# Optimization experiments

Hardware: AMD Instinct MI355X
Metric: run time of the kernel (lower is better)

## Reference

```python
import jax, jax.numpy as jnp
import numpy as np


def setup_inputs() -> dict:
    key = jax.random.key(0)
    ks = jax.random.split(key, 9)
    B, C, H, W = 8, 512, 56, 56
    E = 256  # embed_dim = in_channels / r
    s = 0.02
    return {
        "x": jax.random.normal(ks[0], (B, C, H, W), dtype=jnp.float32),
        "wq": jax.random.normal(ks[1], (E, C), dtype=jnp.float32) * s,
        "bq": jax.random.normal(ks[2], (E,), dtype=jnp.float32) * s,
        "wk": jax.random.normal(ks[3], (E, C), dtype=jnp.float32) * s,
        "bk": jax.random.normal(ks[4], (E,), dtype=jnp.float32) * s,
        "wv": jax.random.normal(ks[5], (E, C), dtype=jnp.float32) * s,
        "bv": jax.random.normal(ks[6], (E,), dtype=jnp.float32) * s,
        "wo": jax.random.normal(ks[7], (C, E), dtype=jnp.float32) * s,
        "bo": jax.random.normal(ks[8], (C,), dtype=jnp.float32) * s,
    }


def reference(x, wq, bq, wk, bk, wv, bv, wo, bo):
    B, C, H, W = x.shape
    N = H * W
    # 1x1 convs == per-pixel linear projections; flatten spatial dims
    xf = x.reshape(B, C, N)                                   # b c n
    q = jnp.einsum("ec,bcn->bne", wq, xf) + bq                # b n e
    k = jnp.einsum("ec,bcn->ben", wk, xf) + bk[None, :, None] # b e n
    v = jnp.einsum("ec,bcn->bne", wv, xf) + bv                # b n e
    attn = jnp.einsum("bne,bem->bnm", q, k) / N               # b n n (unnormalized, /N scale)
    embed = jnp.einsum("bnm,bme->bne", attn, v)               # b n e
    out = jnp.einsum("ce,bne->bcn", wo, embed) + bo[None, :, None]
    return out.reshape(B, C, H, W) + x
```

## Files before the change

kernel.cpp:

```cpp
#include <hip/hip_runtime.h>
#include <hip/hip_bf16.h>


typedef __attribute__((ext_vector_type(8))) __bf16 bf16x8;
typedef __attribute__((ext_vector_type(8))) short s16x8;
typedef __attribute__((ext_vector_type(4))) float floatx4;

struct __align__(8) bh4 { __hip_bfloat16 x, y, z, w; };
struct __align__(16) bh8 { __hip_bfloat16 h[8]; };

__device__ __forceinline__ void load_lds16(const void* g, void* l) {
    __builtin_amdgcn_global_load_lds((const __attribute__((address_space(1))) void*)g,
                                     (__attribute__((address_space(3))) void*)l, 16, 0, 0);
}

__global__ __launch_bounds__(256)
void prep_trans(const float* __restrict__ x, __hip_bfloat16* __restrict__ xnp,
                float* __restrict__ s,
                const float* __restrict__ wo, const float* __restrict__ wv,
                const float* __restrict__ wq, const float* __restrict__ wk,
                const float* __restrict__ bq, const float* __restrict__ bk,
                const float* __restrict__ bv,
                __hip_bfloat16* __restrict__ Pdb, __hip_bfloat16* __restrict__ Qtb,
                float* __restrict__ u, float* __restrict__ r, float* __restrict__ w,
                float* __restrict__ kap)
{
    __shared__ __align__(16) float smem[2 * 16 * 68];
    const int tid = threadIdx.x;

    if (blockIdx.z == 8) {
        const int blk = blockIdx.y * 50 + blockIdx.x;
        if (blk >= 130) return;
        if (blk >= 128) {
            int c = (blk - 128) * 256 + tid;
            float su = 0.f, sr = 0.f, sw = 0.f;
            for (int e = 0; e < 256; ++e) {
                su = fmaf(wo[(long long)c * 256 + e], bv[e], su);
                sr = fmaf(bk[e], wq[(long long)e * 512 + c], sr);
                sw = fmaf(wk[(long long)e * 512 + c], bq[e], sw);
            }
            u[c] = su; r[c] = sr; w[c] = sw;
            if (c == 0) {
                float k2 = 0.f;
                for (int e = 0; e < 256; ++e) k2 = fmaf(bk[e], bq[e], k2);
                *kap = k2;
            }
            return;
        }
        const bool doQ = (blk >= 64);
        const int tt = blk & 63;
        const int m0 = (tt >> 3) * 64, n0 = (tt & 7) * 64;
        float (*As)[68] = (float(*)[68])smem;
        float (*Bs)[68] = (float(*)[68])(smem + 16 * 68);
        const int tx = tid & 15, ty = tid >> 4;
        const int lk = tid >> 4, lc = (tid & 15) * 4;
        const int lr = tid >> 2, lk4 = (tid & 3) * 4;
        float acc[4][4] = {};
        for (int k0 = 0; k0 < 256; k0 += 16) {
            float4 av, bv4;
            if (doQ) {
                av = *(const float4*)&wq[(long long)(k0 + lk) * 512 + m0 + lc];
                bv4 = *(const float4*)&wk[(long long)(k0 + lk) * 512 + n0 + lc];
            } else {
                av = *(const float4*)&wo[(long long)(m0 + lr) * 256 + k0 + lk4];
                bv4 = *(const float4*)&wv[(long long)(k0 + lk) * 512 + n0 + lc];
            }
            __syncthreads();
            if (doQ) {
                *(float4*)&As[lk][lc] = av;
            } else {
                As[lk4 + 0][lr] = av.x; As[lk4 + 1][lr] = av.y;
                As[lk4 + 2][lr] = av.z; As[lk4 + 3][lr] = av.w;
            }
            *(float4*)&Bs[lk][lc] = bv4;
            __syncthreads();
#pragma unroll
            for (int kk = 0; kk < 16; ++kk) {
                float a[4], b[4];
#pragma unroll
                for (int i = 0; i < 4; ++i) { a[i] = As[kk][ty * 4 + i]; b[i] = Bs[kk][tx * 4 + i]; }
#pragma unroll
                for (int i = 0; i < 4; ++i)
#pragma unroll
                    for (int j = 0; j < 4; ++j) acc[i][j] = fmaf(a[i], b[j], acc[i][j]);
            }
        }
        const int mo = m0 + ty * 4, no = n0 + tx * 4;
        if (doQ) {
#pragma unroll
            for (int i = 0; i < 4; ++i)
#pragma unroll
                for (int j = 0; j < 4; ++j)
                    Qtb[(long long)(mo + i) * 512 + no + j] = __float2bfloat16(acc[i][j]);
        } else {
#pragma unroll
            for (int i = 0; i < 4; ++i)
#pragma unroll
                for (int j = 0; j < 4; ++j) {
                    __hip_bfloat16 v = __float2bfloat16(acc[i][j]);
                    Pdb[(long long)(mo + i) * 1024 + no + j] = v;
                    Pdb[(long long)(mo + i) * 1024 + no + j + 512] = v;
                }
        }
        return;
    }

    const int b = blockIdx.z;
    const int n0 = blockIdx.x * 64, c0 = blockIdx.y * 64;
    const int nch = tid & 7;
    const int cr  = tid >> 3;
    __hip_bfloat16* xno = xnp + (long long)b * 512 * 3200;

    if (n0 >= 3136) {
        bh8 z8;
#pragma unroll
        for (int k = 0; k < 8; ++k) z8.h[k] = __float2bfloat16(0.f);
#pragma unroll
        for (int p = 0; p < 2; ++p)
            *(bh8*)&xno[(long long)(c0 + cr + 32 * p) * 3200 + n0 + nch * 8] = z8;
        return;
    }
    const float* xb = x + (long long)b * 512 * 3136;
    float4 v[2][2];
#pragma unroll
    for (int p = 0; p < 2; ++p) {
        const float* xr = xb + (long long)(c0 + cr + 32 * p) * 3136 + n0 + nch * 8;
        v[p][0] = *(const float4*)xr;
        v[p][1] = *(const float4*)(xr + 4);
    }
    float rsum[2];
#pragma unroll
    for (int p = 0; p < 2; ++p) {
        float4 v0 = v[p][0], v1 = v[p][1];
        bh8 o;
        o.h[0] = __float2bfloat16(v0.x); o.h[1] = __float2bfloat16(v0.y);
        o.h[2] = __float2bfloat16(v0.z); o.h[3] = __float2bfloat16(v0.w);
        o.h[4] = __float2bfloat16(v1.x); o.h[5] = __float2bfloat16(v1.y);
        o.h[6] = __float2bfloat16(v1.z); o.h[7] = __float2bfloat16(v1.w);
        *(bh8*)&xno[(long long)(c0 + cr + 32 * p) * 3200 + n0 + nch * 8] = o;
        float rs = v0.x + v0.y + v0.z + v0.w + v1.x + v1.y + v1.z + v1.w;
        rs += __shfl_xor(rs, 1, 8);
        rs += __shfl_xor(rs, 2, 8);
        rs += __shfl_xor(rs, 4, 8);
        rsum[p] = rs;
    }
    if (nch == 0) {
        atomicAdd(&s[b * 512 + c0 + cr], rsum[0]);
        atomicAdd(&s[b * 512 + c0 + cr + 32], rsum[1]);
    }
}

__global__ __launch_bounds__(256)
void vec2_kernel(const __hip_bfloat16* __restrict__ T, const __hip_bfloat16* __restrict__ Pdb,
                 const __hip_bfloat16* __restrict__ Qtb, const float* __restrict__ s,
                 const float* __restrict__ u, const float* __restrict__ w,
                 const float* __restrict__ kap, const float* __restrict__ bo,
                 float* __restrict__ ps, float* __restrict__ sq, float* __restrict__ a2)
{
    const int idx = blockIdx.x * 4 + (threadIdx.x >> 6);
    const int lane = threadIdx.x & 63;
    const int b = idx >> 9, c = idx & 511;
    const int j0 = lane * 8;
    const float* sb = s + b * 512;
    float4 s0 = *(const float4*)&sb[j0], s1 = *(const float4*)&sb[j0 + 4];
    float4 w0 = *(const float4*)&w[j0],  w1 = *(const float4*)&w[j0 + 4];
    bf16x8 pv = *(const bf16x8*)&Pdb[(long long)c * 1024 + j0];
    bf16x8 qv = *(const bf16x8*)&Qtb[(long long)c * 512 + j0];
    bf16x8 tv = *(const bf16x8*)&T[(long long)b * 262144 + (long long)c * 512 + j0];
    float sj[8] = {s0.x, s0.y, s0.z, s0.w, s1.x, s1.y, s1.z, s1.w};
    float wj[8] = {w0.x, w0.y, w0.z, w0.w, w1.x, w1.y, w1.z, w1.w};
    float aps = 0.f, asq = 0.f, atw = 0.f, asw = 0.f;
#pragma unroll
    for (int t = 0; t < 8; ++t) {
        aps = fmaf((float)pv[t], sj[t], aps);
        asq = fmaf((float)qv[t], sj[t], asq);
        atw = fmaf((float)tv[t], wj[t], atw);
        asw = fmaf(sj[t], wj[t], asw);
    }
#pragma unroll
    for (int m = 1; m < 64; m <<= 1) {
        aps += __shfl_xor(aps, m);
        asq += __shfl_xor(asq, m);
        atw += __shfl_xor(atw, m);
        asw += __shfl_xor(asw, m);
    }
    if (lane == 0) {
        ps[idx] = aps; sq[idx] = asq;
        float kp = *kap;
        a2[idx] = (atw + u[c] * asw + aps * kp) * (1.f / 3136.f) + u[c] * kp + bo[c];
    }
}

#define SWZ64(row) ((row) & 7)

__global__ __launch_bounds__(256)
void mfma_g(const __hip_bfloat16* __restrict__ A, long long sA, int lda,
            __hip_bfloat16* __restrict__ C, long long sC, int ldc,
            int kLen)
{
    constexpr int BKT = 64;
    constexpr int CPR = BKT / 8;
    constexpr int NC = 64 * CPR / 256;
    constexpr int LSZ = 64 * BKT;
    __shared__ __hip_bfloat16 As[2 * LSZ];
    __shared__ __hip_bfloat16 Bs[2 * LSZ];
    const int tid = threadIdx.x;
    const int lane = tid & 63;
    const int w = tid >> 6;
    const int wm = (w >> 1) << 5;
    const int wn = (w & 1) << 5;
    const int ln = lane & 15;
    const int hi = lane >> 4;
    const int bx = blockIdx.x;
    const int batch = bx & 7, ks = bx >> 3;
    int p = blockIdx.y, mt = 0;
    while (p >= 8 - mt) { p -= 8 - mt; ++mt; }
    const int nt = mt + p;
    const int m0 = mt << 6, n0 = nt << 6;
    const long long k0 = (long long)ks * kLen;

    const __hip_bfloat16* gA[NC];
    const __hip_bfloat16* gB[NC];
#pragma unroll
    for (int q0 = 0; q0 < NC; ++q0) {
        int q = tid + 256 * q0;
        int row = q / CPR;
        int c = (q % CPR) ^ SWZ64(row);
        gA[q0] = A + batch * sA + (long long)(m0 + row) * lda + k0 + c * 8;
        gB[q0] = A + batch * sA + (long long)(n0 + row) * lda + k0 + c * 8;
    }
    floatx4 acc[2][2] = {};
    const int nK = kLen / BKT;

#pragma unroll
    for (int q0 = 0; q0 < NC; ++q0) {
        load_lds16(gA[q0], As + (tid + 256 * q0) * 8);
        load_lds16(gB[q0], Bs + (tid + 256 * q0) * 8);
        gA[q0] += BKT; gB[q0] += BKT;
    }

    int cur = 0;
    for (int kt = 0; kt < nK; ++kt) {
        if (kt + 1 < nK) {
            const int off = (cur ^ 1) * LSZ;
#pragma unroll
            for (int q0 = 0; q0 < NC; ++q0) {
                load_lds16(gA[q0], As + off + (tid + 256 * q0) * 8);
                load_lds16(gB[q0], Bs + off + (tid + 256 * q0) * 8);
                gA[q0] += BKT; gB[q0] += BKT;
            }
            asm volatile("s_waitcnt vmcnt(4)" ::: "memory");
        } else {
            asm volatile("s_waitcnt vmcnt(0)" ::: "memory");
        }
        __builtin_amdgcn_s_barrier();
        const __hip_bfloat16* Ac = As + cur * LSZ;
        const __hip_bfloat16* Bc = Bs + cur * LSZ;
#pragma unroll
        for (int kk = 0; kk < BKT / 32; ++kk) {
            const int cidx = kk * 4 + hi;
            bf16x8 af[2], bfr[2];
#pragma unroll
            for (int i = 0; i < 2; ++i) {
                int row = wm + i * 16 + ln;
                af[i] = *(const bf16x8*)(Ac + row * BKT + ((cidx ^ SWZ64(row)) << 3));
            }
#pragma unroll
            for (int j = 0; j < 2; ++j) {
                int row = wn + j * 16 + ln;
                bfr[j] = *(const bf16x8*)(Bc + row * BKT + ((cidx ^ SWZ64(row)) << 3));
            }
#pragma unroll
            for (int i = 0; i < 2; ++i)
#pragma unroll
                for (int j = 0; j < 2; ++j)
                    acc[i][j] = __builtin_amdgcn_mfma_f32_16x16x32_bf16(af[i], bfr[j], acc[i][j], 0, 0, 0);
        }
        if (kt + 1 < nK) {
            __builtin_amdgcn_s_barrier();
            cur ^= 1;
        }
    }

    __hip_bfloat16* Cb = C + batch * sC + ks * 512;
#pragma unroll
    for (int i = 0; i < 2; ++i) {
        int mb = m0 + wm + i * 16 + hi * 4;
#pragma unroll
        for (int j = 0; j < 2; ++j) {
            int nl = n0 + wn + j * 16 + ln;
            bh4 mv;
            mv.x = __float2bfloat16(acc[i][j][0]);
            mv.y = __float2bfloat16(acc[i][j][1]);
            mv.z = __float2bfloat16(acc[i][j][2]);
            mv.w = __float2bfloat16(acc[i][j][3]);
            Cb[(long long)(mb + 0) * ldc + nl] = mv.x;
            Cb[(long long)(mb + 1) * ldc + nl] = mv.y;
            Cb[(long long)(mb + 2) * ldc + nl] = mv.z;
            Cb[(long long)(mb + 3) * ldc + nl] = mv.w;
            if (mt != nt)
                *(bh4*)&Cb[(long long)nl * ldc + mb] = mv;
        }
    }
}

template<int MODE>
__global__ __launch_bounds__(256)
void mfma_sm(const __hip_bfloat16* __restrict__ A, long long sA, int lda,
             const __hip_bfloat16* __restrict__ B, long long sB, int ldb,
             __hip_bfloat16* __restrict__ C, long long sC, int ldc,
             const float* __restrict__ pu, const float* __restrict__ pr,
             const float* __restrict__ pps, const float* __restrict__ psq,
             int kLen)
{
    constexpr int BKT = 64;
    constexpr int CPR = BKT / 8;
    constexpr int NC = 64 * CPR / 256;
    constexpr int LSZ = 64 * BKT;
    __shared__ __hip_bfloat16 As[2 * LSZ];
    __shared__ __hip_bfloat16 Bs[2 * LSZ];
    const int tid = threadIdx.x;
    const int lane = tid & 63;
    const int w = tid >> 6;
    const int wm = (w >> 1) << 5;
    const int wn = (w & 1) << 5;
    const int ln = lane & 15;
    const int hi = lane >> 4;
    const int batch = blockIdx.x;
    const int m0 = blockIdx.z << 6;
    const int n0 = blockIdx.y << 6;

    const __hip_bfloat16* gA[NC];
    const __hip_bfloat16* gB[NC];
#pragma unroll
    for (int q0 = 0; q0 < NC; ++q0) {
        int q = tid + 256 * q0;
        int row = q / CPR;
        int c = (q % CPR) ^ SWZ64(row);
        gA[q0] = A + batch * sA + (long long)(m0 + row) * lda + c * 8;
        gB[q0] = B + batch * sB + (long long)(n0 + row) * ldb + c * 8;
    }
    floatx4 acc[2][2] = {};
    const int nK = kLen / BKT;

#pragma unroll
    for (int q0 = 0; q0 < NC; ++q0) {
        load_lds16(gA[q0], As + (tid + 256 * q0) * 8);
        load_lds16(gB[q0], Bs + (tid + 256 * q0) * 8);
        gA[q0] += BKT; gB[q0] += BKT;
    }

    int cur = 0;
    for (int kt = 0; kt < nK; ++kt) {
        if (kt + 1 < nK) {
            const int off = (cur ^ 1) * LSZ;
#pragma unroll
            for (int q0 = 0; q0 < NC; ++q0) {
                load_lds16(gA[q0], As + off + (tid + 256 * q0) * 8);
                load_lds16(gB[q0], Bs + off + (tid + 256 * q0) * 8);
                gA[q0] += BKT; gB[q0] += BKT;
            }
            asm volatile("s_waitcnt vmcnt(4)" ::: "memory");
        } else {
            asm volatile("s_waitcnt vmcnt(0)" ::: "memory");
        }
        __builtin_amdgcn_s_barrier();
        const __hip_bfloat16* Ac = As + cur * LSZ;
        const __hip_bfloat16* Bc = Bs + cur * LSZ;
#pragma unroll
        for (int kk = 0; kk < BKT / 32; ++kk) {
            const int cidx = kk * 4 + hi;
            bf16x8 af[2], bfr[2];
#pragma unroll
            for (int i = 0; i < 2; ++i) {
                int row = wm + i * 16 + ln;
                af[i] = *(const bf16x8*)(Ac + row * BKT + ((cidx ^ SWZ64(row)) << 3));
            }
#pragma unroll
            for (int j = 0; j < 2; ++j) {
                int row = wn + j * 16 + ln;
                bfr[j] = *(const bf16x8*)(Bc + row * BKT + ((cidx ^ SWZ64(row)) << 3));
            }
#pragma unroll
            for (int i = 0; i < 2; ++i)
#pragma unroll
                for (int j = 0; j < 2; ++j)
                    acc[i][j] = __builtin_amdgcn_mfma_f32_16x16x32_bf16(af[i], bfr[j], acc[i][j], 0, 0, 0);
        }
        if (kt + 1 < nK) {
            __builtin_amdgcn_s_barrier();
            cur ^= 1;
        }
    }

    __hip_bfloat16* Cb = C + batch * sC;
#pragma unroll
    for (int i = 0; i < 2; ++i) {
        int mb = m0 + wm + i * 16 + hi * 4;
#pragma unroll
        for (int r = 0; r < 4; ++r) {
#pragma unroll
            for (int j = 0; j < 2; ++j) {
                int nl = n0 + wn + j * 16 + ln;
                float v = acc[i][j][r];
                if (MODE == 6) {
                    float uu = pu[mb + r], rr = pr[nl];
                    v = (v + uu * psq[batch * 512 + nl] + pps[batch * 512 + mb + r] * rr)
                        * (1.f / 3136.f) + uu * rr;
                    if (mb + r == nl) v += 1.f;
                }
                Cb[(long long)(mb + r) * ldc + nl] = __float2bfloat16(v);
            }
        }
    }
}

#define SWZB(nr) (((nr) & 7) ^ (((nr) >> 3) & 7))

__global__ __launch_bounds__(256)
void mfma64(const __hip_bfloat16* __restrict__ A, long long sA, int lda,
            const __hip_bfloat16* __restrict__ Bn, long long sB, int ldb,
            float* __restrict__ C, long long sC, int ldc,
            const float* __restrict__ bias, int sBias,
            int kLen, int Nreal)
{
    constexpr int BKT = 64;
    constexpr int CPR = BKT / 8;
    constexpr int NA = 64 * CPR / 256;
    __shared__ __hip_bfloat16 As[64 * BKT];
    __shared__ __align__(16) short Bs[128 * 64];
    const int tid = threadIdx.x;
    const int lane = tid & 63;
    const int w = tid >> 6;
    const int ln = lane & 15;
    const int hi = lane >> 4;
    const int batch = blockIdx.x;
    const int m0 = blockIdx.z << 6;
    const int n0 = blockIdx.y << 7;

    const __hip_bfloat16* gA[NA];
#pragma unroll
    for (int q0 = 0; q0 < NA; ++q0) {
        int q = tid + 256 * q0;
        int row = q / CPR;
        int c = (q % CPR) ^ SWZ64(row);
        gA[q0] = A + batch * sA + (long long)(m0 + row) * lda + c * 8;
    }
    const int bc = tid >> 2;
    const int bq = tid & 3;
    const short* bbase = (const short*)(Bn + batch * sB)
                         + (long long)bc * ldb + n0 + bq * 8;
    const int g = bc >> 3;

    floatx4 acc[4][2] = {};
    const int nK = kLen / BKT;
    for (int kt = 0; kt < nK; ++kt) {
        s16x8 vb[4];
        const short* bp = bbase + (long long)kt * 64 * ldb;
#pragma unroll
        for (int m = 0; m < 4; ++m)
            vb[m] = *(const s16x8*)(bp + m * 32);
#pragma unroll
        for (int q0 = 0; q0 < NA; ++q0) {
            load_lds16(gA[q0], As + (tid + 256 * q0) * 8);
            gA[q0] += BKT;
        }
#pragma unroll
        for (int m = 0; m < 4; ++m) {
            const int nb = (bq + 4 * m) * 8;
#pragma unroll
            for (int k = 0; k < 8; ++k) {
                const int nr = nb + k;
                Bs[nr * 64 + (((g ^ SWZB(nr)) & 7) << 3) + (bc & 7)] = vb[m][k];
            }
        }
        __syncthreads();
#pragma unroll
        for (int kk = 0; kk < BKT / 32; ++kk) {
            const int cidx = kk * 4 + hi;
            bf16x8 af[4], bfr[2];
#pragma unroll
            for (int i = 0; i < 4; ++i) {
                int row = i * 16 + ln;
                af[i] = *(const bf16x8*)(As + row * BKT + ((cidx ^ SWZ64(row)) << 3));
            }
#pragma unroll
            for (int j = 0; j < 2; ++j) {
                int row = w * 32 + j * 16 + ln;
                bfr[j] = *(const bf16x8*)((const __hip_bfloat16*)Bs
                          + row * 64 + (((cidx ^ SWZB(row)) & 7) << 3));
            }
#pragma unroll
            for (int i = 0; i < 4; ++i)
#pragma unroll
                for (int j = 0; j < 2; ++j)
                    acc[i][j] = __builtin_amdgcn_mfma_f32_16x16x32_bf16(af[i], bfr[j], acc[i][j], 0, 0, 0);
        }
        __syncthreads();
    }

    float* Cb = C + batch * sC;
#pragma unroll
    for (int i = 0; i < 4; ++i) {
        int mb = m0 + i * 16 + hi * 4;
#pragma unroll
        for (int r = 0; r < 4; ++r) {
            float bb = bias[batch * sBias + mb + r];
#pragma unroll
            for (int j = 0; j < 2; ++j) {
                int nl = n0 + w * 32 + j * 16 + ln;
                if (nl < Nreal) {
                    Cb[(long long)(mb + r) * ldc + nl] = acc[i][j][r] + bb;
                }
            }
        }
    }
}

extern "C" void kernel_launch(void* const* d_in, const int* in_sizes, int n_in,
                              void* d_out, int out_size, void* d_ws, size_t ws_size,
                              hipStream_t stream)
{
    const float* x  = (const float*)d_in[0];
    const float* wq = (const float*)d_in[1];
    const float* bq = (const float*)d_in[2];
    const float* wk = (const float*)d_in[3];
    const float* bk = (const float*)d_in[4];
    const float* wv = (const float*)d_in[5];
    const float* bv = (const float*)d_in[6];
    const float* wo = (const float*)d_in[7];
    const float* bo = (const float*)d_in[8];
    float* out = (float*)d_out;

    const int N = 3136;
    const long long xs = 512LL * N;
    const long long xs2 = 512LL * 3200;

    char* ob = (char*)d_out;
    __hip_bfloat16* Gp2 = (__hip_bfloat16*)(ob + 26214400);
    __hip_bfloat16* Tb  = (__hip_bfloat16*)(ob + 34603008);

    char* wsb = (char*)d_ws;
    __hip_bfloat16* xnp = (__hip_bfloat16*)wsb;
    __hip_bfloat16* A2b = (__hip_bfloat16*)(wsb + 26214400);
    __hip_bfloat16* Pdb = (__hip_bfloat16*)(wsb + 30408704);
    __hip_bfloat16* Qtb = (__hip_bfloat16*)(wsb + 31457280);
    float* sv  = (float*)(wsb + 31981568);
    float* u_  = (float*)(wsb + 31997952);
    float* r_  = (float*)(wsb + 32000000);
    float* w_  = (float*)(wsb + 32002048);
    float* kap = (float*)(wsb + 32004096);
    float* ps  = (float*)(wsb + 32004112);
    float* sq  = (float*)(wsb + 32020496);
    float* a2v = (float*)(wsb + 32036880);

    hipMemsetAsync(sv, 0, 512 * 8 * sizeof(float), stream);

    prep_trans<<<dim3(50, 8, 9), 256, 0, stream>>>(
        x, xnp, sv, wo, wv, wq, wk, bq, bk, bv,
        Pdb, Qtb, u_, r_, w_, kap);

    mfma_g<<<dim3(16, 36), 256, 0, stream>>>(
        xnp, xs2, 3200, Gp2, 524288, 1024, 1600);

    mfma_sm<5><<<dim3(8, 8, 8), 256, 0, stream>>>(
        Pdb, 0, 1024, Gp2, 524288, 1024, Tb, 262144, 512,
        nullptr, nullptr, nullptr, nullptr, 1024);

    vec2_kernel<<<1024, 256, 0, stream>>>(Tb, Pdb, Qtb, sv, u_, w_, kap, bo, ps, sq, a2v);

    mfma_sm<6><<<dim3(8, 8, 8), 256, 0, stream>>>(
        Tb, 262144, 512, Qtb, 0, 512, A2b, 262144, 512,
        u_, r_, ps, sq, 512);

    mfma64<<<dim3(8, 25, 8), 256, 0, stream>>>(
        A2b, 262144, 512, xnp, xs2, 3200,
        out, xs, N, a2v, 512, 512, N);
}
```

Measured before the change: 215.7 us.

## Move weight-product GEMMs from conversion kernel into Gram MFMA kernel

Drops the weight-product blocks (Wo·Wv, Wq^T·Wk and the bias vectors) from the x-conversion kernel, leaving it a pure fp32-to-bf16 transpose/convert. Those blocks now run as extra blockIdx.y rows inside the Gram MFMA kernel, sharing one LDS arena, so the weight GEMMs overlap the x-Gram compute instead of the streaming conversion. The fp32 weight GEMM also gets register prefetch of the next k-tile. The conversion kernel loses its tail imbalance, but the merged kernel gains extra blocks and may run at lower occupancy.

```diff
diff --git a/kernel.cpp b/kernel.cpp
--- a/kernel.cpp
+++ b/kernel.cpp
@@ -15,98 +15,12 @@
 }
 
 __global__ __launch_bounds__(256)
-void prep_trans(const float* __restrict__ x, __hip_bfloat16* __restrict__ xnp,
-                float* __restrict__ s,
-                const float* __restrict__ wo, const float* __restrict__ wv,
-                const float* __restrict__ wq, const float* __restrict__ wk,
-                const float* __restrict__ bq, const float* __restrict__ bk,
-                const float* __restrict__ bv,
-                __hip_bfloat16* __restrict__ Pdb, __hip_bfloat16* __restrict__ Qtb,
-                float* __restrict__ u, float* __restrict__ r, float* __restrict__ w,
-                float* __restrict__ kap)
+void conv_x(const float* __restrict__ x, __hip_bfloat16* __restrict__ xnp,
+            float* __restrict__ s)
 {
-    __shared__ __align__(16) float smem[2 * 16 * 68];
-    const int tid = threadIdx.x;
-
-    if (blockIdx.z == 8) {
-        const int blk = blockIdx.y * 50 + blockIdx.x;
-        if (blk >= 130) return;
-        if (blk >= 128) {
-            int c = (blk - 128) * 256 + tid;
-            float su = 0.f, sr = 0.f, sw = 0.f;
-            for (int e = 0; e < 256; ++e) {
-                su = fmaf(wo[(long long)c * 256 + e], bv[e], su);
-                sr = fmaf(bk[e], wq[(long long)e * 512 + c], sr);
-                sw = fmaf(wk[(long long)e * 512 + c], bq[e], sw);
-            }
-            u[c] = su; r[c] = sr; w[c] = sw;
-            if (c == 0) {
-                float k2 = 0.f;
-                for (int e = 0; e < 256; ++e) k2 = fmaf(bk[e], bq[e], k2);
-                *kap = k2;
-            }
-            return;
-        }
-        const bool doQ = (blk >= 64);
-        const int tt = blk & 63;
-        const int m0 = (tt >> 3) * 64, n0 = (tt & 7) * 64;
-        float (*As)[68] = (float(*)[68])smem;
-        float (*Bs)[68] = (float(*)[68])(smem + 16 * 68);
-        const int tx = tid & 15, ty = tid >> 4;
-        const int lk = tid >> 4, lc = (tid & 15) * 4;
-        const int lr = tid >> 2, lk4 = (tid & 3) * 4;
-        float acc[4][4] = {};
-        for (int k0 = 0; k0 < 256; k0 += 16) {
-            float4 av, bv4;
-            if (doQ) {
-                av = *(const float4*)&wq[(long long)(k0 + lk) * 512 + m0 + lc];
-                bv4 = *(const float4*)&wk[(long long)(k0 + lk) * 512 + n0 + lc];
-            } else {
-                av = *(const float4*)&wo[(long long)(m0 + lr) * 256 + k0 + lk4];
-                bv4 = *(const float4*)&wv[(long long)(k0 + lk) * 512 + n0 + lc];
-            }
-            __syncthreads();
-            if (doQ) {
-                *(float4*)&As[lk][lc] = av;
-            } else {
-                As[lk4 + 0][lr] = av.x; As[lk4 + 1][lr] = av.y;
-                As[lk4 + 2][lr] = av.z; As[lk4 + 3][lr] = av.w;
-            }
-            *(float4*)&Bs[lk][lc] = bv4;
-            __syncthreads();
-#pragma unroll
-            for (int kk = 0; kk < 16; ++kk) {
-                float a[4], b[4];
-#pragma unroll
-                for (int i = 0; i < 4; ++i) { a[i] = As[kk][ty * 4 + i]; b[i] = Bs[kk][tx * 4 + i]; }
-#pragma unroll
-                for (int i = 0; i < 4; ++i)
-#pragma unroll
-                    for (int j = 0; j < 4; ++j) acc[i][j] = fmaf(a[i], b[j], acc[i][j]);
-            }
-        }
-        const int mo = m0 + ty * 4, no = n0 + tx * 4;
-        if (doQ) {
-#pragma unroll
-            for (int i = 0; i < 4; ++i)
-#pragma unroll
-                for (int j = 0; j < 4; ++j)
-                    Qtb[(long long)(mo + i) * 512 + no + j] = __float2bfloat16(acc[i][j]);
-        } else {
-#pragma unroll
-            for (int i = 0; i < 4; ++i)
-#pragma unroll
-                for (int j = 0; j < 4; ++j) {
-                    __hip_bfloat16 v = __float2bfloat16(acc[i][j]);
-                    Pdb[(long long)(mo + i) * 1024 + no + j] = v;
-                    Pdb[(long long)(mo + i) * 1024 + no + j + 512] = v;
-                }
-        }
-        return;
-    }
-
     const int b = blockIdx.z;
     const int n0 = blockIdx.x * 64, c0 = blockIdx.y * 64;
+    const int tid = threadIdx.x;
     const int nch = tid & 7;
     const int cr  = tid >> 3;
     __hip_bfloat16* xno = xnp + (long long)b * 512 * 3200;
@@ -194,21 +108,118 @@
 #define SWZ64(row) ((row) & 7)
 
 __global__ __launch_bounds__(256)
-void mfma_g(const __hip_bfloat16* __restrict__ A, long long sA, int lda,
-            __hip_bfloat16* __restrict__ C, long long sC, int ldc,
-            int kLen)
+void mfma_g_w(const __hip_bfloat16* __restrict__ A, long long sA, int lda,
+              __hip_bfloat16* __restrict__ C, long long sC, int ldc, int kLen,
+              const float* __restrict__ wo, const float* __restrict__ wv,
+              const float* __restrict__ wq, const float* __restrict__ wk,
+              const float* __restrict__ bq, const float* __restrict__ bk,
+              const float* __restrict__ bv,
+              __hip_bfloat16* __restrict__ Pdb, __hip_bfloat16* __restrict__ Qtb,
+              float* __restrict__ u, float* __restrict__ r, float* __restrict__ w,
+              float* __restrict__ kap)
 {
     constexpr int BKT = 64;
     constexpr int CPR = BKT / 8;
     constexpr int NC = 64 * CPR / 256;
     constexpr int LSZ = 64 * BKT;
-    __shared__ __hip_bfloat16 As[2 * LSZ];
-    __shared__ __hip_bfloat16 Bs[2 * LSZ];
+    __shared__ __align__(16) char arena[4 * LSZ * 2];
     const int tid = threadIdx.x;
+
+    if (blockIdx.y >= 36) {
+        const int blk = (blockIdx.y - 36) * 16 + blockIdx.x;
+        if (blk >= 130) return;
+        if (blk >= 128) {
+            int c = (blk - 128) * 256 + tid;
+            float su = 0.f, sr = 0.f, sw = 0.f;
+            for (int e = 0; e < 256; ++e) {
+                su = fmaf(wo[(long long)c * 256 + e], bv[e], su);
+                sr = fmaf(bk[e], wq[(long long)e * 512 + c], sr);
+                sw = fmaf(wk[(long long)e * 512 + c], bq[e], sw);
+            }
+            u[c] = su; r[c] = sr; w[c] = sw;
+            if (c == 0) {
+                float k2 = 0.f;
+                for (int e = 0; e < 256; ++e) k2 = fmaf(bk[e], bq[e], k2);
+                *kap = k2;
+            }
+            return;
+        }
+        const bool doQ = (blk >= 64);
+        const int tt = blk & 63;
+        const int m0 = (tt >> 3) * 64, n0 = (tt & 7) * 64;
+        float* smem = (float*)arena;
+        float (*As)[68] = (float(*)[68])smem;
+        float (*Bs)[68] = (float(*)[68])(smem + 16 * 68);
+        const int tx = tid & 15, ty = tid >> 4;
+        const int lk = tid >> 4, lc = (tid & 15) * 4;
+        const int lr = tid >> 2, lk4 = (tid & 3) * 4;
+        float acc[4][4] = {};
+
+        float4 av, bv4, nav, nbv;
+        if (doQ) {
+            av  = *(const float4*)&wq[(long long)lk * 512 + m0 + lc];
+            bv4 = *(const float4*)&wk[(long long)lk * 512 + n0 + lc];
+        } else {
+            av  = *(const float4*)&wo[(long long)(m0 + lr) * 256 + lk4];
+            bv4 = *(const float4*)&wv[(long long)lk * 512 + n0 + lc];
+        }
+        for (int k0 = 0; k0 < 256; k0 += 16) {
+            __syncthreads();
+            if (doQ) {
+                *(float4*)&As[lk][lc] = av;
+            } else {
+                As[lk4 + 0][lr] = av.x; As[lk4 + 1][lr] = av.y;
+                As[lk4 + 2][lr] = av.z; As[lk4 + 3][lr] = av.w;
+            }
+            *(float4*)&Bs[lk][lc] = bv4;
+            __syncthreads();
+            if (k0 + 16 < 256) {
+                if (doQ) {
+                    nav = *(const float4*)&wq[(long long)(k0 + 16 + lk) * 512 + m0 + lc];
+                    nbv = *(const float4*)&wk[(long long)(k0 + 16 + lk) * 512 + n0 + lc];
+                } else {
+                    nav = *(const float4*)&wo[(long long)(m0 + lr) * 256 + k0 + 16 + lk4];
+                    nbv = *(const float4*)&wv[(long long)(k0 + 16 + lk) * 512 + n0 + lc];
+                }
+            }
+#pragma unroll
+            for (int kk = 0; kk < 16; ++kk) {
+                float a[4], b[4];
+#pragma unroll
+                for (int i = 0; i < 4; ++i) { a[i] = As[kk][ty * 4 + i]; b[i] = Bs[kk][tx * 4 + i]; }
+#pragma unroll
+                for (int i = 0; i < 4; ++i)
+#pragma unroll
+                    for (int j = 0; j < 4; ++j) acc[i][j] = fmaf(a[i], b[j], acc[i][j]);
+            }
+            av = nav; bv4 = nbv;
+        }
+        const int mo = m0 + ty * 4, no = n0 + tx * 4;
+        if (doQ) {
+#pragma unroll
+            for (int i = 0; i < 4; ++i)
+#pragma unroll
+                for (int j = 0; j < 4; ++j)
+                    Qtb[(long long)(mo + i) * 512 + no + j] = __float2bfloat16(acc[i][j]);
+        } else {
+#pragma unroll
+            for (int i = 0; i < 4; ++i)
+#pragma unroll
+                for (int j = 0; j < 4; ++j) {
+                    __hip_bfloat16 v = __float2bfloat16(acc[i][j]);
+                    Pdb[(long long)(mo + i) * 1024 + no + j] = v;
+                    Pdb[(long long)(mo + i) * 1024 + no + j + 512] = v;
+                }
+        }
+        return;
+    }
+
+    __hip_bfloat16* As = (__hip_bfloat16*)arena;
+    __hip_bfloat16* Bs = As + 2 * LSZ;
     const int lane = tid & 63;
-    const int w = tid >> 6;
-    const int wm = (w >> 1) << 5;
-    const int wn = (w & 1) << 5;
+    const int wv_ = tid >> 6;
+    const int wm = (wv_ >> 1) << 5;
+    const int wn = (wv_ & 1) << 5;
     const int ln = lane & 15;
     const int hi = lane >> 4;
     const int bx = blockIdx.x;
@@ -556,12 +567,11 @@
 
     hipMemsetAsync(sv, 0, 512 * 8 * sizeof(float), stream);
 
-    prep_trans<<<dim3(50, 8, 9), 256, 0, stream>>>(
-        x, xnp, sv, wo, wv, wq, wk, bq, bk, bv,
-        Pdb, Qtb, u_, r_, w_, kap);
-
-    mfma_g<<<dim3(16, 36), 256, 0, stream>>>(
-        xnp, xs2, 3200, Gp2, 524288, 1024, 1600);
+    conv_x<<<dim3(50, 8, 8), 256, 0, stream>>>(x, xnp, sv);
+
+    mfma_g_w<<<dim3(16, 45), 256, 0, stream>>>(
+        xnp, xs2, 3200, Gp2, 524288, 1024, 1600,
+        wo, wv, wq, wk, bq, bk, bv, Pdb, Qtb, u_, r_, w_, kap);
 
     mfma_sm<5><<<dim3(8, 8, 8), 256, 0, stream>>>(
         Pdb, 0, 1024, Gp2, 524288, 1024, Tb, 262144, 512,
```

New measurement: 209.4 us. -2.9%, faster.
